# Optimization experiments

Measured on AMD Instinct MI355X. Metric: run time of the kernel, lower is better.

Reference implementation:

```python
import jax, jax.numpy as jnp
import numpy as np

N, E, D_IN, H, OUT = 50000, 800000, 128, 256, 2
BN_EPS = 1e-5
LN_EPS = 1e-5


def _xavier(k, fi, fo):
    lim = float(np.sqrt(6.0 / (fi + fo)))
    return jax.random.uniform(k, (fi, fo), minval=-lim, maxval=lim, dtype=jnp.float32)


def setup_inputs() -> dict:
    key = jax.random.key(0)
    ks = jax.random.split(key, 8)
    return {
        "x": jax.random.normal(ks[0], (N, D_IN), dtype=jnp.float32),
        "edge_index": jax.random.randint(ks[1], (2, E), 0, N, dtype=jnp.int32),
        "feature_scale": jnp.ones((D_IN,), jnp.float32),
        "feature_bias": jnp.zeros((D_IN,), jnp.float32),
        "bn0_g": jnp.ones((D_IN,), jnp.float32),
        "bn0_b": jnp.zeros((D_IN,), jnp.float32),
        "W1": _xavier(ks[2], D_IN, H), "b1": jnp.zeros((H,), jnp.float32),
        "bn1_g": jnp.ones((H,), jnp.float32), "bn1_b": jnp.zeros((H,), jnp.float32),
        "ln1_g": jnp.ones((H,), jnp.float32), "ln1_b": jnp.zeros((H,), jnp.float32),
        "W2": _xavier(ks[3], H, H), "b2": jnp.zeros((H,), jnp.float32),
        "bn2_g": jnp.ones((H,), jnp.float32), "bn2_b": jnp.zeros((H,), jnp.float32),
        "ln2_g": jnp.ones((H,), jnp.float32), "ln2_b": jnp.zeros((H,), jnp.float32),
        "Wout": _xavier(ks[4], H, OUT), "bout": jnp.zeros((OUT,), jnp.float32),
    }


def _batchnorm(x, g, b):
    # training-mode BatchNorm1d: batch stats over node axis, biased variance
    mu = jnp.mean(x, axis=0)
    var = jnp.mean(jnp.square(x - mu), axis=0)
    return g * (x - mu) * jax.lax.rsqrt(var + BN_EPS) + b


def _layernorm(x, g, b):
    mu = jnp.mean(x, axis=-1, keepdims=True)
    var = jnp.mean(jnp.square(x - mu), axis=-1, keepdims=True)
    return g * (x - mu) * jax.lax.rsqrt(var + LN_EPS) + b


def _gcn(x, W, b, src, dst, dinv):
    # PyG GCNConv with self-loops: D^{-1/2}(A+I)D^{-1/2} X W + b
    h = x @ W                                   # [N, F]
    norm = (dinv[src] * dinv[dst])[:, None]     # [E, 1]
    msg = h[src] * norm                         # [E, F] (dominant traffic)
    agg = jax.ops.segment_sum(msg, dst, num_segments=N)
    return agg + (dinv * dinv)[:, None] * h + b


def _forward(x, feature_scale, feature_bias, bn0_g, bn0_b,
             W1, b1, bn1_g, bn1_b, ln1_g, ln1_b,
             W2, b2, bn2_g, bn2_b, ln2_g, ln2_b,
             Wout, bout, edge_index):
    src, dst = edge_index[0], edge_index[1]
    deg = jax.ops.segment_sum(jnp.ones((E,), x.dtype), dst, num_segments=N) + 1.0
    dinv = jax.lax.rsqrt(deg)

    h = x * feature_scale + feature_bias
    h = _batchnorm(h, bn0_g, bn0_b)            # input_bn; dropout = identity (eval)

    # layer 0 (no residual: i == 0)
    h1 = _gcn(h, W1, b1, src, dst, dinv)
    h1 = jax.nn.relu(h1)
    h1 = _batchnorm(h1, bn1_g, bn1_b)
    h1 = _layernorm(h1, ln1_g, ln1_b)

    # layer 1 (residual add, shapes match)
    h2 = _gcn(h1, W2, b2, src, dst, dinv)
    h2 = jax.nn.relu(h2)
    h2 = _batchnorm(h2, bn2_g, bn2_b)
    h2 = _layernorm(h2, ln2_g, ln2_b)
    h2 = h2 + h1

    return h2 @ Wout + bout


def reference(x, edge_index, feature_scale, feature_bias, bn0_g, bn0_b,
              W1, b1, bn1_g, bn1_b, ln1_g, ln1_b,
              W2, b2, bn2_g, bn2_b, ln2_g, ln2_b,
              Wout, bout):
    return _forward(x, feature_scale, feature_bias, bn0_g, bn0_b,
                    W1, b1, bn1_g, bn1_b, ln1_g, ln1_b,
                    W2, b2, bn2_g, bn2_b, ln2_g, ln2_b,
                    Wout, bout, edge_index)
```

## Files before the change

kernel.cpp:

```cpp
#include <hip/hip_runtime.h>
#include <hip/hip_bf16.h>
#include <stdint.h>

#define N_NODES 50000
#define N_EDGES 800000
#define D_IN    128
#define H_DIM   256
#define BN_EPS  1e-5f
#define LN_EPS  1e-5f
#define NBLK2 782
#define SLICE_ELEMS ((size_t)N_NODES * 32)
#define EDGE_CHUNK 4096
#define BN0_BLOCKS 256
#define PREPX_BLOCKS 6250
#define TR_BLOCKS 256
#define NBKT 196
#define CHUNK 4096
#define RCHUNKS 196

typedef float v4f __attribute__((ext_vector_type(4)));
typedef short v8s __attribute__((ext_vector_type(8)));
typedef unsigned v4u __attribute__((ext_vector_type(4)));

__device__ __forceinline__ float bflo(unsigned u){ return __uint_as_float(u << 16); }
__device__ __forceinline__ float bfhi(unsigned u){ return __uint_as_float(u & 0xffff0000u); }
__device__ __forceinline__ unsigned short f2bf(float f){
  unsigned u = __float_as_uint(f);
  u += 0x7fffu + ((u >> 16) & 1u);
  return (unsigned short)(u >> 16);
}
__device__ __forceinline__ unsigned pack2(float a, float b){
  return (unsigned)f2bf(a) | ((unsigned)f2bf(b) << 16);
}

__device__ __forceinline__ int block_excl_scan(int v){
  int t = threadIdx.x;
  int lane = t & 63, w = t >> 6;
  int inc = v;
  #pragma unroll
  for (int m = 1; m < 64; m <<= 1){
    int o = __shfl_up(inc, m, 64);
    if (lane >= m) inc += o;
  }
  __shared__ int wsum[4];
  if (lane == 63) wsum[w] = inc;
  __syncthreads();
  int base = 0;
  #pragma unroll
  for (int j = 0; j < 4; ++j) if (j < w) base += wsum[j];
  return base + inc - v;
}

__global__ __launch_bounds__(256) void bn0r1_k(const int* ei, const float* x,
                                               const float* fs, const float* fb,
                                               float* S, float* Q, int* ghist){
  int b = blockIdx.x, t = threadIdx.x;
  if (b >= BN0_BLOCKS){
    __shared__ int lh[NBKT];
    int b2 = b - BN0_BLOCKS;
    for (int i = t; i < NBKT; i += 256) lh[i] = 0;
    __syncthreads();
    int e0 = b2 * CHUNK;
    int n = min(CHUNK, N_EDGES - e0);
    for (int i = t; i < n; i += 256)
      atomicAdd(&lh[ei[N_EDGES + e0 + i] >> 8], 1);
    __syncthreads();
    if (t < NBKT && lh[t] > 0) atomicAdd(&ghist[t], lh[t]);
    return;
  }
  int cl = t & 31, rg = t >> 5;
  int c = cl * 4;
  float4 fs4 = *(const float4*)(fs + c);
  float4 fb4 = *(const float4*)(fb + c);
  float s0=0,s1=0,s2=0,s3=0,q0=0,q1=0,q2=0,q3=0;
  for (int row = b * 8 + rg; row < N_NODES; row += BN0_BLOCKS * 8){
    float4 xv = *(const float4*)(x + (size_t)row * D_IN + c);
    float v0 = xv.x * fs4.x + fb4.x;
    float v1 = xv.y * fs4.y + fb4.y;
    float v2 = xv.z * fs4.z + fb4.z;
    float v3 = xv.w * fs4.w + fb4.w;
    s0 += v0; s1 += v1; s2 += v2; s3 += v3;
    q0 += v0*v0; q1 += v1*v1; q2 += v2*v2; q3 += v3*v3;
  }
  __shared__ float red[256][8];
  red[t][0]=s0; red[t][1]=s1; red[t][2]=s2; red[t][3]=s3;
  red[t][4]=q0; red[t][5]=q1; red[t][6]=q2; red[t][7]=q3;
  __syncthreads();
  float* Sr = S + (b & 3) * D_IN;
  float* Qr = Q + (b & 3) * D_IN;
  if (t < 32){
    float a[8];
    #pragma unroll
    for (int i = 0; i < 8; ++i) a[i] = red[t][i];
    for (int j = 1; j < 8; ++j)
      #pragma unroll
      for (int i = 0; i < 8; ++i) a[i] += red[t + 32*j][i];
    #pragma unroll
    for (int i = 0; i < 4; ++i){ atomicAdd(&Sr[t*4+i], a[i]); atomicAdd(&Qr[t*4+i], a[4+i]); }
  }
}

__global__ __launch_bounds__(256) void r3_k(const int* ei, const int* ghist, int* gcursor, unsigned* ebuf){
  __shared__ unsigned short dstS[CHUNK];
  __shared__ int lh[NBKT], cb[NBKT], sbb[NBKT];
  int t = threadIdx.x;
  int v = (t < NBKT) ? ghist[t] : 0;
  int epre = block_excl_scan(v);
  if (t < NBKT){ sbb[t] = epre; lh[t] = 0; }
  __syncthreads();
  int e0 = blockIdx.x * CHUNK;
  int n = min(CHUNK, N_EDGES - e0);
  for (int i = t; i < n; i += 256){
    int d = ei[N_EDGES + e0 + i];
    dstS[i] = (unsigned short)d;
    atomicAdd(&lh[d >> 8], 1);
  }
  __syncthreads();
  if (t < NBKT && lh[t] > 0) cb[t] = sbb[t] + atomicAdd(&gcursor[t], lh[t]);
  __syncthreads();
  if (t < NBKT) lh[t] = 0;
  __syncthreads();
  for (int i = t; i < n; i += 256){
    int d = dstS[i];
    int bkt = d >> 8;
    int r = atomicAdd(&lh[bkt], 1);
    unsigned src = (unsigned)ei[e0 + i];
    ebuf[cb[bkt] + r] = ((unsigned)(d & 255) << 16) | src;
  }
}

__global__ __launch_bounds__(256) void r4a_k(const unsigned* ebuf, const int* ghist,
                                             int* cnt, int* dhist){
  __shared__ int h[256], dh[128], sbb[NBKT + 1];
  int t = threadIdx.x, b = blockIdx.x;
  int v = (t < NBKT) ? ghist[t] : 0;
  int epre = block_excl_scan(v);
  if (t < NBKT) sbb[t] = epre;
  if (t == NBKT - 1) sbb[NBKT] = epre + v;
  h[t] = 0;
  if (t < 128) dh[t] = 0;
  __syncthreads();
  int lo = sbb[b], hi = sbb[b + 1];
  for (int i = lo + t; i < hi; i += 256)
    atomicAdd(&h[(ebuf[i] >> 16) & 255], 1);
  __syncthreads();
  int node = b * 256 + t;
  if (node < N_NODES){
    cnt[node] = h[t];
    atomicAdd(&dh[min(h[t], 127)], 1);
  }
  __syncthreads();
  if (t < 128 && dh[t] > 0) atomicAdd(&dhist[t], dh[t]);
}

__global__ __launch_bounds__(256) void dperm2_k(const int* cnt, const int* dhist, int* reserve,
                                                int* perm, int* rank, int* offs, float* dinv){
  __shared__ int ep_s[128], W_s[128], lb[128], lh[128], lc[128];
  int t = threadIdx.x;
  int v = (t < 128) ? dhist[t] : 0;
  int e1 = block_excl_scan(v);
  __syncthreads();
  int e2 = block_excl_scan((t < 128) ? v * t : 0);
  __syncthreads();
  if (t < 128){ ep_s[t] = e1; W_s[t] = e2; lh[t] = 0; lc[t] = 0; }
  __syncthreads();
  for (int i = blockIdx.x * 256 + t; i < N_NODES; i += 32 * 256)
    atomicAdd(&lh[min(cnt[i], 127)], 1);
  __syncthreads();
  if (t < 128 && lh[t] > 0) lb[t] = ep_s[t] + atomicAdd(&reserve[t], lh[t]);
  __syncthreads();
  for (int i = blockIdx.x * 256 + t; i < N_NODES; i += 32 * 256){
    int d = cnt[i];
    int b = min(d, 127);
    int r = atomicAdd(&lc[b], 1);
    int pos = lb[b] + r;
    perm[pos] = i;
    rank[i] = pos;
    offs[pos] = W_s[b] + (pos - ep_s[b]) * d;
    dinv[i] = rsqrtf((float)d + 1.0f);
  }
  if (blockIdx.x == 0 && t == 0) offs[N_NODES] = N_EDGES;
}

__global__ __launch_bounds__(256) void r4bprep_k(const unsigned* ebuf, const int* ghist,
                                                 const int* rank, const int* offs,
                                                 unsigned short* edges,
                                                 const float* x, const float* S, const float* Q,
                                                 const float* fs, const float* fb,
                                                 const float* gg, const float* bb,
                                                 unsigned short* xt,
                                                 const float* W1, const float* W2,
                                                 unsigned short* W1t, unsigned short* W2t){
  __shared__ int curs[256], sbb[NBKT + 1];
  int b = blockIdx.x, t = threadIdx.x;
  if (b < NBKT){
    int v = (t < NBKT) ? ghist[t] : 0;
    int epre = block_excl_scan(v);
    if (t < NBKT) sbb[t] = epre;
    if (t == NBKT - 1) sbb[NBKT] = epre + v;
    int node = b * 256 + t;
    if (node < N_NODES) curs[t] = offs[rank[node]];
    __syncthreads();
    int lo = sbb[b], hi = sbb[b + 1];
    for (int i = lo + t; i < hi; i += 256){
      unsigned u = ebuf[i];
      int l8 = (u >> 16) & 255;
      int pos = atomicAdd(&curs[l8], 1);
      edges[pos] = (unsigned short)(u & 0xffffu);
    }
    return;
  }
  if (b < NBKT + PREPX_BLOCKS){
    int i = (b - NBKT) * 256 + t;
    int row = i >> 5; int c = (i & 31) * 4;
    float4 Sv = *(const float4*)(S + c);
    float4 Qv = *(const float4*)(Q + c);
    #pragma unroll
    for (int rep = 1; rep < 4; ++rep){
      float4 s2 = *(const float4*)(S + rep * D_IN + c);
      float4 q2 = *(const float4*)(Q + rep * D_IN + c);
      Sv.x += s2.x; Sv.y += s2.y; Sv.z += s2.z; Sv.w += s2.w;
      Qv.x += q2.x; Qv.y += q2.y; Qv.z += q2.z; Qv.w += q2.w;
    }
    float4 fs4 = *(const float4*)(fs + c);
    float4 fb4 = *(const float4*)(fb + c);
    float4 gg4 = *(const float4*)(gg + c);
    float4 bb4 = *(const float4*)(bb + c);
    const float invN = 1.0f / N_NODES;
    float mu0 = Sv.x*invN, mu1 = Sv.y*invN, mu2 = Sv.z*invN, mu3 = Sv.w*invN;
    float r0 = rsqrtf(Qv.x*invN - mu0*mu0 + BN_EPS);
    float r1 = rsqrtf(Qv.y*invN - mu1*mu1 + BN_EPS);
    float r2 = rsqrtf(Qv.z*invN - mu2*mu2 + BN_EPS);
    float r3 = rsqrtf(Qv.w*invN - mu3*mu3 + BN_EPS);
    float a0 = gg4.x*r0*fs4.x, c0 = gg4.x*r0*(fb4.x - mu0) + bb4.x;
    float a1 = gg4.y*r1*fs4.y, c1 = gg4.y*r1*(fb4.y - mu1) + bb4.y;
    float a2 = gg4.z*r2*fs4.z, c2 = gg4.z*r2*(fb4.z - mu2) + bb4.z;
    float a3 = gg4.w*r3*fs4.w, c3 = gg4.w*r3*(fb4.w - mu3) + bb4.w;
    float4 xv = *(const float4*)(x + (size_t)row * D_IN + c);
    uint2 o;
    o.x = pack2(a0 * xv.x + c0, a1 * xv.y + c1);
    o.y = pack2(a2 * xv.z + c2, a3 * xv.w + c3);
    *(uint2*)(xt + (size_t)row * D_IN + c) = o;
    return;
  }
  int i = (b - NBKT - PREPX_BLOCKS) * 256 + t;
  if (i < D_IN * H_DIM){
    int r = i / H_DIM, c = i % H_DIM;
    W1t[c * D_IN + r] = f2bf(W1[i]);
  }
  if (i < H_DIM * H_DIM){
    int r = i / H_DIM, c = i % H_DIM;
    W2t[c * H_DIM + r] = f2bf(W2[i]);
  }
}

template<int K>
__global__ __launch_bounds__(256) void gemm_k(const unsigned short* A, const unsigned short* Bt,
                                              const float* dinv, unsigned short* C, int M){
  __shared__ __align__(16) short smem[16896];
  __shared__ float dvs[64];
  short* As = smem;
  short* Bs = smem + 64 * 40;
  int t = threadIdx.x;
  int m0 = blockIdx.x * 64;
  int lane = t & 63;
  int w = t >> 6;
  int fr = lane & 15, quad = lane >> 4;
  if (t < 64) dvs[t] = (m0 + t < M) ? dinv[m0 + t] : 0.0f;
  v4f acc[4][4] = {};
  int sr = t >> 2;
  int sk = (t & 3) << 3;
  for (int k0 = 0; k0 < K; k0 += 32){
    __syncthreads();
    uint4 av = {0,0,0,0};
    int arow = m0 + sr;
    if (arow < M) av = *(const uint4*)(A + (size_t)arow * K + k0 + sk);
    *(uint4*)(&As[sr * 40 + sk]) = av;
    #pragma unroll
    for (int j = 0; j < 4; ++j){
      int brow = sr + 64 * j;
      uint4 bv = *(const uint4*)(Bt + (size_t)brow * K + k0 + sk);
      *(uint4*)(&Bs[brow * 40 + sk]) = bv;
    }
    __syncthreads();
    v8s af[4], bf[4];
    #pragma unroll
    for (int mi = 0; mi < 4; ++mi)
      af[mi] = *(const v8s*)(&As[(mi * 16 + fr) * 40 + quad * 8]);
    #pragma unroll
    for (int ni = 0; ni < 4; ++ni)
      bf[ni] = *(const v8s*)(&Bs[(w * 64 + ni * 16 + fr) * 40 + quad * 8]);
    #pragma unroll
    for (int mi = 0; mi < 4; ++mi)
      #pragma unroll
      for (int ni = 0; ni < 4; ++ni)
        acc[mi][ni] = __builtin_amdgcn_mfma_f32_16x16x32_bf16(af[mi], bf[ni], acc[mi][ni], 0, 0, 0);
  }
  __syncthreads();
  short* Cs = smem;
  #pragma unroll
  for (int mi = 0; mi < 4; ++mi)
    #pragma unroll
    for (int ni = 0; ni < 4; ++ni)
      #pragma unroll
      for (int r = 0; r < 4; ++r){
        int row = mi * 16 + quad * 4 + r;
        int col = w * 64 + ni * 16 + fr;
        Cs[row * 264 + col] = (short)f2bf(acc[mi][ni][r] * dvs[row]);
      }
  __syncthreads();
  int orow = t >> 2;
  int grow = m0 + orow;
  if (grow < M){
    #pragma unroll
    for (int j = 0; j < 4; ++j){
      int oc = (t & 3) * 16 + 64 * j;
      v8s v0 = *(const v8s*)(&Cs[orow * 264 + oc]);
      v8s v1 = *(const v8s*)(&Cs[orow * 264 + oc + 8]);
      *(v8s*)(&C[(size_t)(oc >> 5) * SLICE_ELEMS + (size_t)grow * 32 + (oc & 31)]) = v0;
      int oc1 = oc + 8;
      *(v8s*)(&C[(size_t)(oc1 >> 5) * SLICE_ELEMS + (size_t)grow * 32 + (oc1 & 31)]) = v1;
    }
  }
}

#define ACC8(vv) { a0 += bflo(vv.x); a1 += bfhi(vv.x); a2 += bflo(vv.y); a3 += bfhi(vv.y); \
                   a4 += bflo(vv.z); a5 += bfhi(vv.z); a6 += bflo(vv.w); a7 += bfhi(vv.w); }

__global__ __launch_bounds__(256) void agg_k(const unsigned short* hs, const int* offsets,
                                             const unsigned short* edges, const int* perm,
                                             const float* dinv, const float* bias,
                                             unsigned short* g, float* pS, float* pQ){
  __shared__ unsigned eds32[EDGE_CHUNK / 2];
  __shared__ float wps[4][4][16];
  int t = threadIdx.x;
  int lane = t & 63;
  int wv = t >> 6;
  int slice = blockIdx.x & 7;
  int l4 = lane & 3;
  int grp = NBLK2 - 1 - (blockIdx.x >> 3);
  int nb = grp * 64;
  int idx = nb + (t >> 2);
  int lastn = min(nb + 64, N_NODES);
  int blk0 = offsets[nb];
  int base = blk0 & ~1;
  int blkN = offsets[lastn];
  const unsigned* gsrc = (const unsigned*)(edges + base);
  int nu = min((blkN - base + 1) >> 1, EDGE_CHUNK / 2);
  for (int i = t; i < nu; i += 256)
    eds32[i] = gsrc[i];
  __syncthreads();
  bool act = idx < N_NODES;
  int node = act ? perm[idx] : 0;
  float dv = act ? dinv[node] : 0.f;
  const uint4* hb4 = (const uint4*)(hs + (size_t)slice * SLICE_ELEMS);
  float4 bb0 = *(const float4*)(bias + slice * 32 + l4 * 8);
  float4 bb1 = *(const float4*)(bias + slice * 32 + l4 * 8 + 4);
  uint4 sv = hb4[(size_t)node * 4 + l4];
  float a0 = bflo(sv.x), a1 = bfhi(sv.x);
  float a2 = bflo(sv.y), a3 = bfhi(sv.y);
  float a4 = bflo(sv.z), a5 = bfhi(sv.z);
  float a6 = bflo(sv.w), a7 = bfhi(sv.w);
  int e  = act ? offsets[idx] : 0;
  int e1 = act ? offsets[idx + 1] : 0;
  if ((e & 1) && e < e1){
    int ru = (e - base) >> 1;
    unsigned d = (ru < EDGE_CHUNK / 2) ? eds32[ru] : gsrc[ru];
    uint4 vv = hb4[(size_t)(d >> 16) * 4 + l4];
    ACC8(vv);
    ++e;
  }
  for (; e + 16 <= e1; e += 16){
    int ru = (e - base) >> 1;
    unsigned dd[8];
    if (ru + 8 <= EDGE_CHUNK / 2){
      #pragma unroll
      for (int j = 0; j < 8; ++j) dd[j] = eds32[ru + j];
    } else {
      #pragma unroll
      for (int j = 0; j < 8; ++j) dd[j] = gsrc[ru + j];
    }
    uint4 v[16];
    #pragma unroll
    for (int j = 0; j < 8; ++j){
      v[2*j]   = hb4[(size_t)(dd[j] & 0xffffu) * 4 + l4];
      v[2*j+1] = hb4[(size_t)(dd[j] >> 16)     * 4 + l4];
    }
    #pragma unroll
    for (int j = 0; j < 16; ++j) ACC8(v[j]);
  }
  if (e + 8 <= e1){
    int ru = (e - base) >> 1;
    unsigned dd[4];
    if (ru + 4 <= EDGE_CHUNK / 2){
      #pragma unroll
      for (int j = 0; j < 4; ++j) dd[j] = eds32[ru + j];
    } else {
      #pragma unroll
      for (int j = 0; j < 4; ++j) dd[j] = gsrc[ru + j];
    }
    uint4 v[8];
    #pragma unroll
    for (int j = 0; j < 4; ++j){
      v[2*j]   = hb4[(size_t)(dd[j] & 0xffffu) * 4 + l4];
      v[2*j+1] = hb4[(size_t)(dd[j] >> 16)     * 4 + l4];
    }
    #pragma unroll
    for (int j = 0; j < 8; ++j) ACC8(v[j]);
    e += 8;
  }
  if (e + 4 <= e1){
    int ru = (e - base) >> 1;
    unsigned dd[2];
    if (ru + 2 <= EDGE_CHUNK / 2){
      dd[0] = eds32[ru]; dd[1] = eds32[ru + 1];
    } else {
      dd[0] = gsrc[ru]; dd[1] = gsrc[ru + 1];
    }
    uint4 v[4];
    #pragma unroll
    for (int j = 0; j < 2; ++j){
      v[2*j]   = hb4[(size_t)(dd[j] & 0xffffu) * 4 + l4];
      v[2*j+1] = hb4[(size_t)(dd[j] >> 16)     * 4 + l4];
    }
    #pragma unroll
    for (int j = 0; j < 4; ++j) ACC8(v[j]);
    e += 4;
  }
  for (; e < e1; ++e){
    int r = e - base;
    unsigned d = ((r >> 1) < EDGE_CHUNK / 2) ? eds32[r >> 1] : gsrc[r >> 1];
    unsigned s = (r & 1) ? (d >> 16) : (d & 0xffffu);
    uint4 vv = hb4[(size_t)s * 4 + l4];
    ACC8(vv);
  }
  float y0 = act ? fmaxf(dv * a0 + bb0.x, 0.f) : 0.f;
  float y1 = act ? fmaxf(dv * a1 + bb0.y, 0.f) : 0.f;
  float y2 = act ? fmaxf(dv * a2 + bb0.z, 0.f) : 0.f;
  float y3 = act ? fmaxf(dv * a3 + bb0.w, 0.f) : 0.f;
  float y4 = act ? fmaxf(dv * a4 + bb1.x, 0.f) : 0.f;
  float y5 = act ? fmaxf(dv * a5 + bb1.y, 0.f) : 0.f;
  float y6 = act ? fmaxf(dv * a6 + bb1.z, 0.f) : 0.f;
  float y7 = act ? fmaxf(dv * a7 + bb1.w, 0.f) : 0.f;
  if (act){
    v4u o;
    o.x = pack2(y0, y1); o.y = pack2(y2, y3);
    o.z = pack2(y4, y5); o.w = pack2(y6, y7);
    __builtin_nontemporal_store(o, (v4u*)(g + (size_t)node * H_DIM + slice * 32 + l4 * 8));
  }
  float q0 = y0*y0, q1 = y1*y1, q2 = y2*y2, q3 = y3*y3;
  float q4 = y4*y4, q5 = y5*y5, q6 = y6*y6, q7 = y7*y7;
  #pragma unroll
  for (int m = 4; m < 64; m <<= 1){
    y0 += __shfl_xor(y0, m, 64); y1 += __shfl_xor(y1, m, 64);
    y2 += __shfl_xor(y2, m, 64); y3 += __shfl_xor(y3, m, 64);
    y4 += __shfl_xor(y4, m, 64); y5 += __shfl_xor(y5, m, 64);
    y6 += __shfl_xor(y6, m, 64); y7 += __shfl_xor(y7, m, 64);
    q0 += __shfl_xor(q0, m, 64); q1 += __shfl_xor(q1, m, 64);
    q2 += __shfl_xor(q2, m, 64); q3 += __shfl_xor(q3, m, 64);
    q4 += __shfl_xor(q4, m, 64); q5 += __shfl_xor(q5, m, 64);
    q6 += __shfl_xor(q6, m, 64); q7 += __shfl_xor(q7, m, 64);
  }
  if (lane < 4){
    wps[wv][lane][0] = y0; wps[wv][lane][1] = y1; wps[wv][lane][2] = y2; wps[wv][lane][3] = y3;
    wps[wv][lane][4] = y4; wps[wv][lane][5] = y5; wps[wv][lane][6] = y6; wps[wv][lane][7] = y7;
    wps[wv][lane][8] = q0; wps[wv][lane][9] = q1; wps[wv][lane][10] = q2; wps[wv][lane][11] = q3;
    wps[wv][lane][12] = q4; wps[wv][lane][13] = q5; wps[wv][lane][14] = q6; wps[wv][lane][15] = q7;
  }
  __syncthreads();
  if (t < 64){
    int tl = t >> 4, ti = t & 15;
    float v = wps[0][tl][ti] + wps[1][tl][ti] + wps[2][tl][ti] + wps[3][tl][ti];
    int col32 = tl * 8 + (ti & 7);
    if (ti < 8) pS[(size_t)blockIdx.x * 32 + col32] = v;
    else        pQ[(size_t)blockIdx.x * 32 + col32] = v;
  }
}

__global__ __launch_bounds__(1024) void redu_k(const float* pS, const float* pQ,
                                               const float* gg, const float* bb,
                                               float* sc, float* sh){
  __shared__ float ls[32][32], lq[32][32];
  int t = threadIdx.x;
  int slice = blockIdx.x;
  int grp = t >> 5, c32 = t & 31;
  float as = 0.f, aq = 0.f;
  for (int blk2 = grp; blk2 < NBLK2; blk2 += 32){
    size_t o = ((size_t)blk2 * 8 + slice) * 32 + c32;
    as += pS[o]; aq += pQ[o];
  }
  ls[grp][c32] = as; lq[grp][c32] = aq;
  __syncthreads();
  if (t < 32){
    float S = 0.f, Q = 0.f;
    #pragma unroll
    for (int gI = 0; gI < 32; ++gI){ S += ls[gI][t]; Q += lq[gI][t]; }
    int col = slice * 32 + t;
    const float invN = 1.0f / N_NODES;
    float mu = S * invN;
    float rs = rsqrtf(Q * invN - mu * mu + BN_EPS);
    float s = gg[col] * rs;
    sc[col] = s;
    sh[col] = bb[col] - s * mu;
  }
}

__global__ __launch_bounds__(256) void apply1_k(const unsigned short* g, const float* sc, const float* sh,
                                                const float* lng, const float* lnb, unsigned short* h1){
  int t = threadIdx.x;
  int lane32 = t & 31;
  int row = blockIdx.x * 8 + (t >> 5);
  if (row >= N_NODES) return;
  int c = lane32 * 8;
  float4 s40 = *(const float4*)(sc + c);
  float4 s41 = *(const float4*)(sc + c + 4);
  float4 h40 = *(const float4*)(sh + c);
  float4 h41 = *(const float4*)(sh + c + 4);
  uint4 u = *(const uint4*)(g + (size_t)row * H_DIM + c);
  float v0 = s40.x * bflo(u.x) + h40.x;
  float v1 = s40.y * bfhi(u.x) + h40.y;
  float v2 = s40.z * bflo(u.y) + h40.z;
  float v3 = s40.w * bfhi(u.y) + h40.w;
  float v4 = s41.x * bflo(u.z) + h41.x;
  float v5 = s41.y * bfhi(u.z) + h41.y;
  float v6 = s41.z * bflo(u.w) + h41.z;
  float v7 = s41.w * bfhi(u.w) + h41.w;
  float sum = v0+v1+v2+v3+v4+v5+v6+v7;
  float sq  = v0*v0+v1*v1+v2*v2+v3*v3+v4*v4+v5*v5+v6*v6+v7*v7;
  #pragma unroll
  for (int m = 1; m < 32; m <<= 1){ sum += __shfl_xor(sum, m, 64); sq += __shfl_xor(sq, m, 64); }
  float mu = sum * (1.0f / H_DIM);
  float var = sq * (1.0f / H_DIM) - mu * mu;
  float rs = rsqrtf(var + LN_EPS);
  float4 g40 = *(const float4*)(lng + c);
  float4 g41 = *(const float4*)(lng + c + 4);
  float4 b40 = *(const float4*)(lnb + c);
  float4 b41 = *(const float4*)(lnb + c + 4);
  uint4 o;
  o.x = pack2(g40.x * (v0 - mu) * rs + b40.x, g40.y * (v1 - mu) * rs + b40.y);
  o.y = pack2(g40.z * (v2 - mu) * rs + b40.z, g40.w * (v3 - mu) * rs + b40.w);
  o.z = pack2(g41.x * (v4 - mu) * rs + b41.x, g41.y * (v5 - mu) * rs + b41.y);
  o.w = pack2(g41.z * (v6 - mu) * rs + b41.z, g41.w * (v7 - mu) * rs + b41.w);
  *(uint4*)(h1 + (size_t)row * H_DIM + c) = o;
}

__global__ __launch_bounds__(256) void apply2_k(const unsigned short* g, const float* sc, const float* sh,
                                                const float* lng, const float* lnb,
                                                const unsigned short* h1, const float* Wout,
                                                const float* bout, float* out){
  int t = threadIdx.x;
  int lane32 = t & 31;
  int row = blockIdx.x * 8 + (t >> 5);
  if (row >= N_NODES) return;
  int c = lane32 * 8;
  float4 s40 = *(const float4*)(sc + c);
  float4 s41 = *(const float4*)(sc + c + 4);
  float4 h40 = *(const float4*)(sh + c);
  float4 h41 = *(const float4*)(sh + c + 4);
  uint4 u = *(const uint4*)(g + (size_t)row * H_DIM + c);
  float v0 = s40.x * bflo(u.x) + h40.x;
  float v1 = s40.y * bfhi(u.x) + h40.y;
  float v2 = s40.z * bflo(u.y) + h40.z;
  float v3 = s40.w * bfhi(u.y) + h40.w;
  float v4 = s41.x * bflo(u.z) + h41.x;
  float v5 = s41.y * bfhi(u.z) + h41.y;
  float v6 = s41.z * bflo(u.w) + h41.z;
  float v7 = s41.w * bfhi(u.w) + h41.w;
  float sum = v0+v1+v2+v3+v4+v5+v6+v7;
  float sq  = v0*v0+v1*v1+v2*v2+v3*v3+v4*v4+v5*v5+v6*v6+v7*v7;
  #pragma unroll
  for (int m = 1; m < 32; m <<= 1){ sum += __shfl_xor(sum, m, 64); sq += __shfl_xor(sq, m, 64); }
  float mu = sum * (1.0f / H_DIM);
  float var = sq * (1.0f / H_DIM) - mu * mu;
  float rs = rsqrtf(var + LN_EPS);
  float4 g40 = *(const float4*)(lng + c);
  float4 g41 = *(const float4*)(lng + c + 4);
  float4 b40 = *(const float4*)(lnb + c);
  float4 b41 = *(const float4*)(lnb + c + 4);
  uint4 hr = *(const uint4*)(h1 + (size_t)row * H_DIM + c);
  float y0 = g40.x * (v0 - mu) * rs + b40.x + bflo(hr.x);
  float y1 = g40.y * (v1 - mu) * rs + b40.y + bfhi(hr.x);
  float y2 = g40.z * (v2 - mu) * rs + b40.z + bflo(hr.y);
  float y3 = g40.w * (v3 - mu) * rs + b40.w + bfhi(hr.y);
  float y4 = g41.x * (v4 - mu) * rs + b41.x + bflo(hr.z);
  float y5 = g41.y * (v5 - mu) * rs + b41.y + bfhi(hr.z);
  float y6 = g41.z * (v6 - mu) * rs + b41.z + bflo(hr.w);
  float y7 = g41.w * (v7 - mu) * rs + b41.w + bfhi(hr.w);
  float4 w0 = *(const float4*)(Wout + c * 2);
  float4 w1 = *(const float4*)(Wout + c * 2 + 4);
  float4 w2 = *(const float4*)(Wout + c * 2 + 8);
  float4 w3 = *(const float4*)(Wout + c * 2 + 12);
  float o0 = y0*w0.x + y1*w0.z + y2*w1.x + y3*w1.z + y4*w2.x + y5*w2.z + y6*w3.x + y7*w3.z;
  float o1 = y0*w0.y + y1*w0.w + y2*w1.y + y3*w1.w + y4*w2.y + y5*w2.w + y6*w3.y + y7*w3.w;
  #pragma unroll
  for (int m = 1; m < 32; m <<= 1){ o0 += __shfl_xor(o0, m, 64); o1 += __shfl_xor(o1, m, 64); }
  if (lane32 == 0){
    out[(size_t)row * 2 + 0] = o0 + bout[0];
    out[(size_t)row * 2 + 1] = o1 + bout[1];
  }
}

extern "C" void kernel_launch(void* const* d_in, const int* in_sizes, int n_in,
                              void* d_out, int out_size, void* d_ws, size_t ws_size,
                              hipStream_t stream) {
  const float* x    = (const float*)d_in[0];
  const int*   ei   = (const int*)d_in[1];
  const float* fs   = (const float*)d_in[2];
  const float* fb   = (const float*)d_in[3];
  const float* bn0g = (const float*)d_in[4];
  const float* bn0b = (const float*)d_in[5];
  const float* W1   = (const float*)d_in[6];
  const float* b1   = (const float*)d_in[7];
  const float* bn1g = (const float*)d_in[8];
  const float* bn1b = (const float*)d_in[9];
  const float* ln1g = (const float*)d_in[10];
  const float* ln1b = (const float*)d_in[11];
  const float* W2   = (const float*)d_in[12];
  const float* b2   = (const float*)d_in[13];
  const float* bn2g = (const float*)d_in[14];
  const float* bn2b = (const float*)d_in[15];
  const float* ln2g = (const float*)d_in[16];
  const float* ln2b = (const float*)d_in[17];
  const float* Wout = (const float*)d_in[18];
  const float* bout = (const float*)d_in[19];
  float* out = (float*)d_out;

  char* w = (char*)d_ws;
  float* bn0S  = (float*)(w + 0);
  float* bn0Q  = (float*)(w + 2048);
  int*   dhist = (int*)(w + 4096);
  int*   reserve = (int*)(w + 4608);
  int*   ghist  = (int*)(w + 5120);
  int*   gcursor= (int*)(w + 5904);
  const size_t ZERO_BYTES = 6688;
  float* sc1   = (float*)(w + 7488);
  float* sh1   = (float*)(w + 8512);
  float* sc2   = (float*)(w + 9536);
  float* sh2   = (float*)(w + 10560);
  int*   cnt   = (int*)(w + 11584);
  float* dinv  = (float*)(w + 211584);
  int*   offs  = (int*)(w + 411584);
  int*   perm  = (int*)(w + 611712);
  int*   rank  = (int*)(w + 811712);
  unsigned short* edges = (unsigned short*)(w + 1011712);
  unsigned short* xt   = (unsigned short*)(w + 2611712);
  unsigned short* W1t  = (unsigned short*)(w + 15411712);
  unsigned short* W2t  = (unsigned short*)(w + 15477248);
  unsigned short* hlin = (unsigned short*)(w + 15608320);
  unsigned*       ebuf = (unsigned*)(w + 15608320);
  unsigned short* gbuf = (unsigned short*)(w + 41208320);
  unsigned short* h1   = (unsigned short*)(w + 66808320);
  float* pS    = (float*)(w + 92408320);
  float* pQ    = (float*)(w + 94008832);

  (void)in_sizes; (void)n_in; (void)out_size; (void)ws_size;

  hipMemsetAsync(d_ws, 0, ZERO_BYTES, stream);

  bn0r1_k<<<BN0_BLOCKS + RCHUNKS, 256, 0, stream>>>(ei, x, fs, fb, bn0S, bn0Q, ghist);
  r3_k<<<RCHUNKS, 256, 0, stream>>>(ei, ghist, gcursor, ebuf);
  r4a_k<<<NBKT, 256, 0, stream>>>(ebuf, ghist, cnt, dhist);
  dperm2_k<<<32, 256, 0, stream>>>(cnt, dhist, reserve, perm, rank, offs, dinv);
  r4bprep_k<<<NBKT + PREPX_BLOCKS + TR_BLOCKS, 256, 0, stream>>>(
      ebuf, ghist, rank, offs, edges, x, bn0S, bn0Q, fs, fb, bn0g, bn0b, xt, W1, W2, W1t, W2t);

  int ggrid = (N_NODES + 63) / 64;
  int agg_blocks = NBLK2 * 8;

  gemm_k<D_IN><<<ggrid, 256, 0, stream>>>(xt, W1t, dinv, hlin, N_NODES);
  agg_k<<<agg_blocks, 256, 0, stream>>>(hlin, offs, edges, perm, dinv, b1, gbuf, pS, pQ);
  redu_k<<<8, 1024, 0, stream>>>(pS, pQ, bn1g, bn1b, sc1, sh1);
  apply1_k<<<(N_NODES + 7) / 8, 256, 0, stream>>>(gbuf, sc1, sh1, ln1g, ln1b, h1);

  gemm_k<H_DIM><<<ggrid, 256, 0, stream>>>(h1, W2t, dinv, hlin, N_NODES);
  agg_k<<<agg_blocks, 256, 0, stream>>>(hlin, offs, edges, perm, dinv, b2, gbuf, pS, pQ);
  redu_k<<<8, 1024, 0, stream>>>(pS, pQ, bn2g, bn2b, sc2, sh2);
  apply2_k<<<(N_NODES + 7) / 8, 256, 0, stream>>>(gbuf, sc2, sh2, ln2g, ln2b, h1, Wout, bout, out);
}
```

Before: 341.4 us.

## Fuse degree count and permutation into per-bucket local sort; tweak agg kernel

Merges the degree histogram and global degree-sort kernels into one kernel that sorts nodes by degree only within each 256-node bucket, removing a launch and the global reserve atomics and cnt array. Doubles the number of radix chunks by halving the chunk size. The aggregation kernel switches to packed two-float accumulators, adds a min-occupancy launch bound, and walks node groups in forward order rather than reverse. Local-only sorting weakens degree load balance across aggregation blocks, and the occupancy hint may force register spills.

Result: no change. 340.7 us (-0.2%).

```diff
diff --git a/kernel.cpp b/kernel.cpp
--- a/kernel.cpp
+++ b/kernel.cpp
@@ -15,10 +15,11 @@
 #define PREPX_BLOCKS 6250
 #define TR_BLOCKS 256
 #define NBKT 196
-#define CHUNK 4096
-#define RCHUNKS 196
+#define CHUNK 2048
+#define RCHUNKS 391
 
 typedef float v4f __attribute__((ext_vector_type(4)));
+typedef float v2f __attribute__((ext_vector_type(2)));
 typedef short v8s __attribute__((ext_vector_type(8)));
 typedef unsigned v4u __attribute__((ext_vector_type(4)));
 
@@ -129,57 +130,44 @@
   }
 }
 
-__global__ __launch_bounds__(256) void r4a_k(const unsigned* ebuf, const int* ghist,
-                                             int* cnt, int* dhist){
-  __shared__ int h[256], dh[128], sbb[NBKT + 1];
+__global__ __launch_bounds__(256) void dloc_k(const unsigned* ebuf, const int* ghist,
+                                              int* perm, int* rank, int* offs, float* dinv){
+  __shared__ int h[256], dh[128], ep_s[128], W_s[128], lc[128], sbb[NBKT + 1];
   int t = threadIdx.x, b = blockIdx.x;
-  int v = (t < NBKT) ? ghist[t] : 0;
-  int epre = block_excl_scan(v);
-  if (t < NBKT) sbb[t] = epre;
-  if (t == NBKT - 1) sbb[NBKT] = epre + v;
+  int gv = (t < NBKT) ? ghist[t] : 0;
+  int gpre = block_excl_scan(gv);
+  if (t < NBKT) sbb[t] = gpre;
+  if (t == NBKT - 1) sbb[NBKT] = gpre + gv;
   h[t] = 0;
-  if (t < 128) dh[t] = 0;
+  if (t < 128){ dh[t] = 0; lc[t] = 0; }
   __syncthreads();
   int lo = sbb[b], hi = sbb[b + 1];
   for (int i = lo + t; i < hi; i += 256)
     atomicAdd(&h[(ebuf[i] >> 16) & 255], 1);
   __syncthreads();
   int node = b * 256 + t;
-  if (node < N_NODES){
-    cnt[node] = h[t];
-    atomicAdd(&dh[min(h[t], 127)], 1);
-  }
-  __syncthreads();
-  if (t < 128 && dh[t] > 0) atomicAdd(&dhist[t], dh[t]);
-}
-
-__global__ __launch_bounds__(256) void dperm2_k(const int* cnt, const int* dhist, int* reserve,
-                                                int* perm, int* rank, int* offs, float* dinv){
-  __shared__ int ep_s[128], W_s[128], lb[128], lh[128], lc[128];
-  int t = threadIdx.x;
-  int v = (t < 128) ? dhist[t] : 0;
-  int e1 = block_excl_scan(v);
-  __syncthreads();
-  int e2 = block_excl_scan((t < 128) ? v * t : 0);
-  __syncthreads();
-  if (t < 128){ ep_s[t] = e1; W_s[t] = e2; lh[t] = 0; lc[t] = 0; }
-  __syncthreads();
-  for (int i = blockIdx.x * 256 + t; i < N_NODES; i += 32 * 256)
-    atomicAdd(&lh[min(cnt[i], 127)], 1);
-  __syncthreads();
-  if (t < 128 && lh[t] > 0) lb[t] = ep_s[t] + atomicAdd(&reserve[t], lh[t]);
-  __syncthreads();
-  for (int i = blockIdx.x * 256 + t; i < N_NODES; i += 32 * 256){
-    int d = cnt[i];
-    int b = min(d, 127);
-    int r = atomicAdd(&lc[b], 1);
-    int pos = lb[b] + r;
-    perm[pos] = i;
-    rank[i] = pos;
-    offs[pos] = W_s[b] + (pos - ep_s[b]) * d;
-    dinv[i] = rsqrtf((float)d + 1.0f);
-  }
-  if (blockIdx.x == 0 && t == 0) offs[N_NODES] = N_EDGES;
+  bool valid = node < N_NODES;
+  int deg = valid ? h[t] : 0;
+  if (valid) atomicAdd(&dh[min(deg, 127)], 1);
+  __syncthreads();
+  int cv = (t < 128) ? dh[t] : 0;
+  int e1 = block_excl_scan(cv);
+  __syncthreads();
+  int e2 = block_excl_scan((t < 128) ? cv * t : 0);
+  __syncthreads();
+  if (t < 128){ ep_s[t] = e1; W_s[t] = e2; }
+  __syncthreads();
+  if (valid){
+    int bin = min(deg, 127);
+    int r = atomicAdd(&lc[bin], 1);
+    int pl = ep_s[bin] + r;
+    int pos = b * 256 + pl;
+    perm[pos] = node;
+    rank[node] = pos;
+    offs[pos] = lo + W_s[bin] + (pl - ep_s[bin]) * deg;
+    dinv[node] = rsqrtf((float)deg + 1.0f);
+  }
+  if (b == 0 && t == 0) offs[N_NODES] = N_EDGES;
 }
 
 __global__ __launch_bounds__(256) void r4bprep_k(const unsigned* ebuf, const int* ghist,
@@ -324,13 +312,13 @@
   }
 }
 
-#define ACC8(vv) { a0 += bflo(vv.x); a1 += bfhi(vv.x); a2 += bflo(vv.y); a3 += bfhi(vv.y); \
-                   a4 += bflo(vv.z); a5 += bfhi(vv.z); a6 += bflo(vv.w); a7 += bfhi(vv.w); }
-
-__global__ __launch_bounds__(256) void agg_k(const unsigned short* hs, const int* offsets,
-                                             const unsigned short* edges, const int* perm,
-                                             const float* dinv, const float* bias,
-                                             unsigned short* g, float* pS, float* pQ){
+#define ACCP(u, A) { v2f d_ = {bflo(u), bfhi(u)}; A += d_; }
+#define ACC8(vv) ACCP(vv.x, A0) ACCP(vv.y, A1) ACCP(vv.z, A2) ACCP(vv.w, A3)
+
+__global__ __launch_bounds__(256, 4) void agg_k(const unsigned short* hs, const int* offsets,
+                                                const unsigned short* edges, const int* perm,
+                                                const float* dinv, const float* bias,
+                                                unsigned short* g, float* pS, float* pQ){
   __shared__ unsigned eds32[EDGE_CHUNK / 2];
   __shared__ float wps[4][4][16];
   int t = threadIdx.x;
@@ -338,7 +326,7 @@
   int wv = t >> 6;
   int slice = blockIdx.x & 7;
   int l4 = lane & 3;
-  int grp = NBLK2 - 1 - (blockIdx.x >> 3);
+  int grp = blockIdx.x >> 3;
   int nb = grp * 64;
   int idx = nb + (t >> 2);
   int lastn = min(nb + 64, N_NODES);
@@ -352,15 +340,15 @@
   __syncthreads();
   bool act = idx < N_NODES;
   int node = act ? perm[idx] : 0;
-  float dv = act ? dinv[node] : 0.f;
+  float dvv = act ? dinv[node] : 0.f;
   const uint4* hb4 = (const uint4*)(hs + (size_t)slice * SLICE_ELEMS);
   float4 bb0 = *(const float4*)(bias + slice * 32 + l4 * 8);
   float4 bb1 = *(const float4*)(bias + slice * 32 + l4 * 8 + 4);
   uint4 sv = hb4[(size_t)node * 4 + l4];
-  float a0 = bflo(sv.x), a1 = bfhi(sv.x);
-  float a2 = bflo(sv.y), a3 = bfhi(sv.y);
-  float a4 = bflo(sv.z), a5 = bfhi(sv.z);
-  float a6 = bflo(sv.w), a7 = bfhi(sv.w);
+  v2f A0 = {bflo(sv.x), bfhi(sv.x)};
+  v2f A1 = {bflo(sv.y), bfhi(sv.y)};
+  v2f A2 = {bflo(sv.z), bfhi(sv.z)};
+  v2f A3 = {bflo(sv.w), bfhi(sv.w)};
   int e  = act ? offsets[idx] : 0;
   int e1 = act ? offsets[idx + 1] : 0;
   if ((e & 1) && e < e1){
@@ -387,7 +375,7 @@
       v[2*j+1] = hb4[(size_t)(dd[j] >> 16)     * 4 + l4];
     }
     #pragma unroll
-    for (int j = 0; j < 16; ++j) ACC8(v[j]);
+    for (int j = 0; j < 16; ++j){ ACC8(v[j]); }
   }
   if (e + 8 <= e1){
     int ru = (e - base) >> 1;
@@ -406,7 +394,7 @@
       v[2*j+1] = hb4[(size_t)(dd[j] >> 16)     * 4 + l4];
     }
     #pragma unroll
-    for (int j = 0; j < 8; ++j) ACC8(v[j]);
+    for (int j = 0; j < 8; ++j){ ACC8(v[j]); }
     e += 8;
   }
   if (e + 4 <= e1){
@@ -424,7 +412,7 @@
       v[2*j+1] = hb4[(size_t)(dd[j] >> 16)     * 4 + l4];
     }
     #pragma unroll
-    for (int j = 0; j < 4; ++j) ACC8(v[j]);
+    for (int j = 0; j < 4; ++j){ ACC8(v[j]); }
     e += 4;
   }
   for (; e < e1; ++e){
@@ -434,14 +422,14 @@
     uint4 vv = hb4[(size_t)s * 4 + l4];
     ACC8(vv);
   }
-  float y0 = act ? fmaxf(dv * a0 + bb0.x, 0.f) : 0.f;
-  float y1 = act ? fmaxf(dv * a1 + bb0.y, 0.f) : 0.f;
-  float y2 = act ? fmaxf(dv * a2 + bb0.z, 0.f) : 0.f;
-  float y3 = act ? fmaxf(dv * a3 + bb0.w, 0.f) : 0.f;
-  float y4 = act ? fmaxf(dv * a4 + bb1.x, 0.f) : 0.f;
-  float y5 = act ? fmaxf(dv * a5 + bb1.y, 0.f) : 0.f;
-  float y6 = act ? fmaxf(dv * a6 + bb1.z, 0.f) : 0.f;
-  float y7 = act ? fmaxf(dv * a7 + bb1.w, 0.f) : 0.f;
+  float y0 = act ? fmaxf(dvv * A0.x + bb0.x, 0.f) : 0.f;
+  float y1 = act ? fmaxf(dvv * A0.y + bb0.y, 0.f) : 0.f;
+  float y2 = act ? fmaxf(dvv * A1.x + bb0.z, 0.f) : 0.f;
+  float y3 = act ? fmaxf(dvv * A1.y + bb0.w, 0.f) : 0.f;
+  float y4 = act ? fmaxf(dvv * A2.x + bb1.x, 0.f) : 0.f;
+  float y5 = act ? fmaxf(dvv * A2.y + bb1.y, 0.f) : 0.f;
+  float y6 = act ? fmaxf(dvv * A3.x + bb1.z, 0.f) : 0.f;
+  float y7 = act ? fmaxf(dvv * A3.y + bb1.w, 0.f) : 0.f;
   if (act){
     v4u o;
     o.x = pack2(y0, y1); o.y = pack2(y2, y3);
@@ -628,8 +616,6 @@
   char* w = (char*)d_ws;
   float* bn0S  = (float*)(w + 0);
   float* bn0Q  = (float*)(w + 2048);
-  int*   dhist = (int*)(w + 4096);
-  int*   reserve = (int*)(w + 4608);
   int*   ghist  = (int*)(w + 5120);
   int*   gcursor= (int*)(w + 5904);
   const size_t ZERO_BYTES = 6688;
@@ -637,7 +623,6 @@
   float* sh1   = (float*)(w + 8512);
   float* sc2   = (float*)(w + 9536);
   float* sh2   = (float*)(w + 10560);
-  int*   cnt   = (int*)(w + 11584);
   float* dinv  = (float*)(w + 211584);
   int*   offs  = (int*)(w + 411584);
   int*   perm  = (int*)(w + 611712);
@@ -659,8 +644,7 @@
 
   bn0r1_k<<<BN0_BLOCKS + RCHUNKS, 256, 0, stream>>>(ei, x, fs, fb, bn0S, bn0Q, ghist);
   r3_k<<<RCHUNKS, 256, 0, stream>>>(ei, ghist, gcursor, ebuf);
-  r4a_k<<<NBKT, 256, 0, stream>>>(ebuf, ghist, cnt, dhist);
-  dperm2_k<<<32, 256, 0, stream>>>(cnt, dhist, reserve, perm, rank, offs, dinv);
+  dloc_k<<<NBKT, 256, 0, stream>>>(ebuf, ghist, perm, rank, offs, dinv);
   r4bprep_k<<<NBKT + PREPX_BLOCKS + TR_BLOCKS, 256, 0, stream>>>(
       ebuf, ghist, rank, offs, edges, x, bn0S, bn0Q, fs, fb, bn0g, bn0b, xt, W1, W2, W1t, W2t);
 
```
